# Kernel optimization log

Hardware: AMD Instinct MI355X
Metric: run time of the kernel (lower is better)

The kernel has to match this reference:

```python
import jax, jax.numpy as jnp
import numpy as np

B, S, DM, H, HD, M = 2, 1024, 1024, 16, 64, 32  # batch, seq, d_model, heads, head_dim, retrieved
EPS = 1e-5


def setup_inputs() -> dict:
    key = jax.random.key(0)
    ks = jax.random.split(key, 8)
    w = lambda k, shp: (jax.random.normal(k, shp) * 0.02).astype(jnp.float32)
    return {
        "previous_hidden": jax.random.normal(ks[0], (B, S, DM), jnp.float32),
        "mem_kv": jax.random.normal(ks[1], (B, S, M, 2, DM), jnp.float32),  # retrieved [k,v] from knn_memory.search
        "g_val": jax.random.uniform(ks[2], (1,), jnp.float32),
        "ln1_g": jnp.ones((DM,), jnp.float32), "ln1_b": jnp.zeros((DM,), jnp.float32),
        "c_attn_w": w(ks[3], (DM, 3 * DM)), "c_attn_b": jnp.zeros((3 * DM,), jnp.float32),
        "c_proj_w": w(ks[4], (DM, DM)), "c_proj_b": jnp.zeros((DM,), jnp.float32),
        "ln2_g": jnp.ones((DM,), jnp.float32), "ln2_b": jnp.zeros((DM,), jnp.float32),
        "fc_w": w(ks[5], (DM, 4 * DM)), "fc_b": jnp.zeros((4 * DM,), jnp.float32),
        "proj_w": w(ks[6], (4 * DM, DM)), "proj_b": jnp.zeros((DM,), jnp.float32),
    }


def _ln(x, g, b):
    m = jnp.mean(x, -1, keepdims=True)
    v = jnp.mean(jnp.square(x - m), -1, keepdims=True)
    return (x - m) * jax.lax.rsqrt(v + EPS) * g + b


def _split(t):  # [b,s,(h d)] -> [b,h,s,d]
    return t.reshape(B, S, H, HD).transpose(0, 2, 1, 3)


def _merge(t):  # [b,h,s,d] -> [b,s,(h d)]
    return t.transpose(0, 2, 1, 3).reshape(B, S, DM)


def _forward(previous_hidden, mem_kv, g_val, ln1_g, ln1_b, c_attn_w, c_attn_b,
             c_proj_w, c_proj_b, ln2_g, ln2_b, fc_w, fc_b, proj_w, proj_b):
    residual = previous_hidden
    h = _ln(previous_hidden, ln1_g, ln1_b)
    qkv = h @ c_attn_w + c_attn_b
    q, k, v = jnp.split(qkv, 3, axis=-1)
    q, k, v = _split(q), _split(k), _split(v)  # [b,h,s,d]

    # --- memory attention over retrieved k/v (per query position, M candidates) ---
    mem_k = mem_kv[..., 0, :].reshape(B, S, M, H, HD).transpose(0, 3, 1, 2, 4)  # [b,h,s,m,d]
    mem_v = mem_kv[..., 1, :].reshape(B, S, M, H, HD).transpose(0, 3, 1, 2, 4)
    mw = jnp.einsum('bhsd,bhsmd->bhsm', q, mem_k) / jnp.sqrt(jnp.asarray(HD, q.dtype))
    mw = jax.nn.softmax(mw, axis=-1)
    mem_attn_output = _merge(jnp.einsum('bhsm,bhsmd->bhsd', mw, mem_v))  # pre-c_proj (source overwrites c_proj'd output)

    # --- standard causal self-attention (GPT-2 block attn, incl. its c_proj) ---
    scores = jnp.einsum('bhqd,bhkd->bhqk', q, k) / jnp.sqrt(jnp.asarray(HD, q.dtype))
    causal = jnp.tril(jnp.ones((S, S), bool))
    scores = jnp.where(causal, scores, jnp.finfo(scores.dtype).min)
    p = jax.nn.softmax(scores, axis=-1)
    std_attn_output = _merge(jnp.einsum('bhqk,bhkd->bhqd', p, v)) @ c_proj_w + c_proj_b

    # gated combine (apply_linear_g=True, scalar g path since g_val.shape[0]==1)
    attn_output = (1.0 - g_val) * std_attn_output + g_val * mem_attn_output

    h = attn_output + residual
    residual2 = h
    h2 = _ln(h, ln2_g, ln2_b)
    ff = jax.nn.gelu(h2 @ fc_w + fc_b, approximate=True) @ proj_w + proj_b  # gelu_new
    return residual2 + ff


def reference(previous_hidden, mem_kv, g_val, ln1_g, ln1_b, c_attn_w, c_attn_b,
              c_proj_w, c_proj_b, ln2_g, ln2_b, fc_w, fc_b, proj_w, proj_b):
    return _forward(previous_hidden, mem_kv, g_val, ln1_g, ln1_b, c_attn_w, c_attn_b,
                    c_proj_w, c_proj_b, ln2_g, ln2_b, fc_w, fc_b, proj_w, proj_b)
```

## Files before the change

kernel.cpp:

```cpp
#include <hip/hip_runtime.h>


typedef short bf16x8 __attribute__((ext_vector_type(8)));
typedef float f32x4 __attribute__((ext_vector_type(4)));

__device__ __forceinline__ unsigned short f2b(float x) {
  unsigned int u = __float_as_uint(x);
  u += 0x7fffu + ((u >> 16) & 1u);
  return (unsigned short)(u >> 16);
}
__device__ __forceinline__ float b2f(unsigned int bits16) {
  return __uint_as_float(bits16 << 16);
}
__device__ __forceinline__ void async16(const void* g, void* l) {
  __builtin_amdgcn_global_load_lds((__attribute__((address_space(1))) void*)g,
                                   (__attribute__((address_space(3))) void*)l,
                                   16, 0, 0);
}

__global__ __launch_bounds__(256) void transpose_cast_kernel(
    const float* __restrict__ W, unsigned short* __restrict__ Wt, int K, int N) {
  __shared__ float tile[32][33];
  int n0 = blockIdx.x * 32, k0 = blockIdx.y * 32;
  int tx = threadIdx.x, ty = threadIdx.y;
#pragma unroll
  for (int i = 0; i < 4; i++)
    tile[ty + 8 * i][tx] = W[(size_t)(k0 + ty + 8 * i) * N + n0 + tx];
  __syncthreads();
#pragma unroll
  for (int i = 0; i < 4; i++)
    Wt[(size_t)(n0 + ty + 8 * i) * K + k0 + tx] = f2b(tile[tx][ty + 8 * i]);
}

__global__ __launch_bounds__(256) void ln_cast_kernel(
    const float* __restrict__ x, const float* __restrict__ gw,
    const float* __restrict__ bw, unsigned short* __restrict__ out) {
  int row = blockIdx.x, t = threadIdx.x;
  size_t base = (size_t)row * 1024 + t * 4;
  float4 v = *(const float4*)(x + base);
  float s = v.x + v.y + v.z + v.w;
  float q = v.x * v.x + v.y * v.y + v.z * v.z + v.w * v.w;
#pragma unroll
  for (int off = 32; off; off >>= 1) {
    s += __shfl_xor(s, off);
    q += __shfl_xor(q, off);
  }
  __shared__ float red[8];
  int w = t >> 6, l = t & 63;
  if (l == 0) { red[w] = s; red[w + 4] = q; }
  __syncthreads();
  s = red[0] + red[1] + red[2] + red[3];
  q = red[4] + red[5] + red[6] + red[7];
  float mean = s * (1.0f / 1024.0f);
  float var = q * (1.0f / 1024.0f) - mean * mean;
  float rstd = rsqrtf(var + 1e-5f);
  float4 g4 = *(const float4*)(gw + t * 4);
  float4 b4 = *(const float4*)(bw + t * 4);
  out[base + 0] = f2b((v.x - mean) * rstd * g4.x + b4.x);
  out[base + 1] = f2b((v.y - mean) * rstd * g4.y + b4.y);
  out[base + 2] = f2b((v.z - mean) * rstd * g4.z + b4.z);
  out[base + 3] = f2b((v.w - mean) * rstd * g4.w + b4.w);
}

template <int BM, int BN, int MODE>
__global__ __launch_bounds__(256, 2) void gemm_bf16(
    const unsigned short* __restrict__ A, const unsigned short* __restrict__ Bt,
    const float* __restrict__ bias, const float* __restrict__ res,
    void* __restrict__ outp, int N, int K) {
  constexpr int SM = BM / 32, SN = BN / 32;
  __shared__ __align__(16) unsigned short At[BM * 32];
  __shared__ __align__(16) unsigned short Bs[BN * 32];
  const int t = threadIdx.x, w = t >> 6, l = t & 63;
  const int wm = w >> 1, wn = w & 1;
  const int lq = l & 15, lk = l >> 4;
  const int m0 = blockIdx.y * BM, n0 = blockIdx.x * BN;
  const int lr = l >> 2, lc = l & 3;
  const unsigned short* Ag = A + (size_t)(m0 + w * 16 + lr) * K + lc * 8;
  const unsigned short* Bg = Bt + (size_t)(n0 + w * 16 + lr) * K + lc * 8;
  unsigned short* Al = &At[(size_t)t * 8];
  unsigned short* Bl = &Bs[(size_t)t * 8];
  f32x4 acc[SM][SN] = {};

  for (int k0 = 0; k0 < K; k0 += 32) {
#pragma unroll
    for (int p = 0; p < BM / 64; ++p)
      async16(Ag + (size_t)(p * 64) * K + k0, Al + p * 2048);
#pragma unroll
    for (int p = 0; p < BN / 64; ++p)
      async16(Bg + (size_t)(p * 64) * K + k0, Bl + p * 2048);
    __syncthreads();
    bf16x8 af[SM], bv[SN];
#pragma unroll
    for (int i = 0; i < SM; i++)
      af[i] = *(const bf16x8*)&At[(wm * (BM / 2) + i * 16 + lq) * 32 + lk * 8];
#pragma unroll
    for (int j = 0; j < SN; j++)
      bv[j] = *(const bf16x8*)&Bs[(wn * (BN / 2) + j * 16 + lq) * 32 + lk * 8];
#pragma unroll
    for (int i = 0; i < SM; i++)
#pragma unroll
      for (int j = 0; j < SN; j++)
        acc[i][j] = __builtin_amdgcn_mfma_f32_16x16x32_bf16(af[i], bv[j], acc[i][j], 0, 0, 0);
    __syncthreads();
  }

#pragma unroll
  for (int i = 0; i < SM; i++) {
    int mrow = m0 + wm * (BM / 2) + i * 16 + lk * 4;
#pragma unroll
    for (int j = 0; j < SN; j++) {
      int ncol = n0 + wn * (BN / 2) + j * 16 + lq;
      float bval = bias[ncol];
#pragma unroll
      for (int r = 0; r < 4; r++) {
        size_t idx = (size_t)(mrow + r) * N + ncol;
        float v = acc[i][j][r] + bval;
        if (MODE == 0) {
          ((unsigned short*)outp)[idx] = f2b(v);
        } else if (MODE == 1) {
          ((float*)outp)[idx] = v;
        } else if (MODE == 2) {
          float u = v + 0.044715f * v * v * v;
          float e = __expf(1.5957691216057308f * u);
          float th = 1.0f - 2.0f / (e + 1.0f);
          ((unsigned short*)outp)[idx] = f2b(0.5f * v * (1.0f + th));
        } else {
          ((float*)outp)[idx] = v + res[idx];
        }
      }
    }
  }
}

__global__ __launch_bounds__(512) void memattn_kernel(
    const unsigned short* __restrict__ qkv, const float* __restrict__ memkv,
    float* __restrict__ out) {
  int bs = blockIdx.x, t = threadIdx.x;
  __shared__ float qs[1024];
  __shared__ float wsm[512];
  {
    unsigned int u = *(const unsigned int*)(qkv + (size_t)bs * 3072 + t * 2);
    qs[t * 2] = b2f(u & 0xffffu);
    qs[t * 2 + 1] = b2f(u >> 16);
  }
  __syncthreads();
  int h = t >> 5, m = t & 31;
  const float* kp = memkv + (size_t)bs * 65536 + (size_t)m * 2048 + h * 64;
  float dot = 0.0f;
#pragma unroll
  for (int d4 = 0; d4 < 16; ++d4) {
    float4 kk = *(const float4*)(kp + d4 * 4);
    float4 q4 = *(const float4*)(&qs[h * 64 + d4 * 4]);
    dot += kk.x * q4.x + kk.y * q4.y + kk.z * q4.z + kk.w * q4.w;
  }
  dot *= 0.125f;
  float mx = dot;
#pragma unroll
  for (int off = 1; off < 32; off <<= 1) mx = fmaxf(mx, __shfl_xor(mx, off));
  float e = __expf(dot - mx);
  float sm = e;
#pragma unroll
  for (int off = 1; off < 32; off <<= 1) sm += __shfl_xor(sm, off);
  wsm[t] = e / sm;
  __syncthreads();
  const float* vbase = memkv + (size_t)bs * 65536 + 1024;
#pragma unroll
  for (int rep = 0; rep < 2; ++rep) {
    int eidx = t + rep * 512;
    int he = eidx >> 6;
    const float* wrow = &wsm[he * 32];
    float acc = 0.0f;
#pragma unroll
    for (int mm = 0; mm < 32; ++mm) acc += wrow[mm] * vbase[(size_t)mm * 2048 + eidx];
    out[(size_t)bs * 1024 + eidx] = acc;
  }
}

__global__ __launch_bounds__(256) void flash_kernel(
    const unsigned short* __restrict__ qkv, unsigned short* __restrict__ out) {
  int blk = blockIdx.x;
  int qt = blk & 15, bh = blk >> 4;
  int b = bh >> 4, h = bh & 15;
  int t = threadIdx.x, w = t >> 6, l = t & 63;
  int lq = l & 15, lk = l >> 4;
  __shared__ __align__(16) unsigned short Kt[32 * 72];
  __shared__ __align__(16) unsigned short Vt[64 * 40];
  __shared__ __align__(16) unsigned short Pb[4][16 * 40];

  const unsigned short* base = qkv + (size_t)b * 1024 * 3072;
  int qr0 = qt * 64 + w * 16;

  bf16x8 qf0 = *(const bf16x8*)(base + (size_t)(qr0 + lq) * 3072 + h * 64 + lk * 8);
  bf16x8 qf1 = *(const bf16x8*)(base + (size_t)(qr0 + lq) * 3072 + h * 64 + 32 + lk * 8);

  f32x4 o[4] = {};
  float mrow[4], lrow[4];
#pragma unroll
  for (int r = 0; r < 4; r++) { mrow[r] = -1e30f; lrow[r] = 0.0f; }

  int nch = (qt + 1) * 2;
  for (int c = 0; c < nch; ++c) {
    int kv0 = c * 32;
    {
      int rr = t >> 3, d8 = t & 7;
      const unsigned short* krow = base + (size_t)(kv0 + rr) * 3072 + 1024 + h * 64;
      *(bf16x8*)&Kt[rr * 72 + d8 * 8] = *(const bf16x8*)(krow + d8 * 8);
      bf16x8 v8 = *(const bf16x8*)(krow + 1024 + d8 * 8);
#pragma unroll
      for (int i = 0; i < 8; i++) Vt[(d8 * 8 + i) * 40 + rr] = (unsigned short)v8[i];
    }
    __syncthreads();

    f32x4 sv[2];
#pragma unroll
    for (int j = 0; j < 2; j++) {
      if (kv0 + j * 16 <= qr0 + 15) {
        bf16x8 k0f = *(const bf16x8*)&Kt[(j * 16 + lq) * 72 + lk * 8];
        bf16x8 k1f = *(const bf16x8*)&Kt[(j * 16 + lq) * 72 + 32 + lk * 8];
        f32x4 s = {};
        s = __builtin_amdgcn_mfma_f32_16x16x32_bf16(qf0, k0f, s, 0, 0, 0);
        s = __builtin_amdgcn_mfma_f32_16x16x32_bf16(qf1, k1f, s, 0, 0, 0);
#pragma unroll
        for (int r = 0; r < 4; r++) {
          float x = s[r] * 0.125f;
          int qrow = qr0 + lk * 4 + r;
          int kvg = kv0 + j * 16 + lq;
          if (kvg > qrow) x = -1e30f;
          s[r] = x;
        }
        sv[j] = s;
      } else {
        sv[j] = (f32x4){-1e30f, -1e30f, -1e30f, -1e30f};
      }
    }
#pragma unroll
    for (int r = 0; r < 4; r++) {
      float mnew = fmaxf(sv[0][r], sv[1][r]);
#pragma unroll
      for (int off = 1; off < 16; off <<= 1) mnew = fmaxf(mnew, __shfl_xor(mnew, off));
      mnew = fmaxf(mnew, mrow[r]);
      float a = __expf(mrow[r] - mnew);
      float e0 = __expf(sv[0][r] - mnew);
      float e1 = __expf(sv[1][r] - mnew);
      float rs = e0 + e1;
#pragma unroll
      for (int off = 1; off < 16; off <<= 1) rs += __shfl_xor(rs, off);
      lrow[r] = lrow[r] * a + rs;
      mrow[r] = mnew;
      o[0][r] *= a; o[1][r] *= a; o[2][r] *= a; o[3][r] *= a;
      Pb[w][(lk * 4 + r) * 40 + lq] = f2b(e0);
      Pb[w][(lk * 4 + r) * 40 + 16 + lq] = f2b(e1);
    }
    __syncthreads();

    if (kv0 <= qr0 + 15) {
      bf16x8 pf = *(const bf16x8*)&Pb[w][lq * 40 + lk * 8];
#pragma unroll
      for (int dt = 0; dt < 4; dt++) {
        bf16x8 vf = *(const bf16x8*)&Vt[(dt * 16 + lq) * 40 + lk * 8];
        o[dt] = __builtin_amdgcn_mfma_f32_16x16x32_bf16(pf, vf, o[dt], 0, 0, 0);
      }
    }
    __syncthreads();
  }

  unsigned short* op = out + (size_t)b * 1024 * 1024 + h * 64;
#pragma unroll
  for (int dt = 0; dt < 4; dt++)
#pragma unroll
    for (int r = 0; r < 4; r++) {
      float v = o[dt][r] / lrow[r];
      op[(size_t)(qr0 + lk * 4 + r) * 1024 + dt * 16 + lq] = f2b(v);
    }
}

__global__ __launch_bounds__(256) void combine_ln2_kernel(
    const float* __restrict__ stdp, const float* __restrict__ mem,
    const float* __restrict__ resid, const float* __restrict__ gval,
    const float* __restrict__ gw, const float* __restrict__ bw,
    float* __restrict__ hmid, unsigned short* __restrict__ h2) {
  int row = blockIdx.x, t = threadIdx.x;
  float g = gval[0];
  size_t base = (size_t)row * 1024 + t * 4;
  float4 a = *(const float4*)(stdp + base);
  float4 m4 = *(const float4*)(mem + base);
  float4 r4 = *(const float4*)(resid + base);
  float4 hv;
  hv.x = (1.0f - g) * a.x + g * m4.x + r4.x;
  hv.y = (1.0f - g) * a.y + g * m4.y + r4.y;
  hv.z = (1.0f - g) * a.z + g * m4.z + r4.z;
  hv.w = (1.0f - g) * a.w + g * m4.w + r4.w;
  *(float4*)(hmid + base) = hv;
  float s = hv.x + hv.y + hv.z + hv.w;
  float q = hv.x * hv.x + hv.y * hv.y + hv.z * hv.z + hv.w * hv.w;
#pragma unroll
  for (int off = 32; off; off >>= 1) {
    s += __shfl_xor(s, off);
    q += __shfl_xor(q, off);
  }
  __shared__ float red[8];
  int w = t >> 6, l = t & 63;
  if (l == 0) { red[w] = s; red[w + 4] = q; }
  __syncthreads();
  s = red[0] + red[1] + red[2] + red[3];
  q = red[4] + red[5] + red[6] + red[7];
  float mean = s * (1.0f / 1024.0f);
  float var = q * (1.0f / 1024.0f) - mean * mean;
  float rstd = rsqrtf(var + 1e-5f);
  float4 g4 = *(const float4*)(gw + t * 4);
  float4 b4 = *(const float4*)(bw + t * 4);
  h2[base + 0] = f2b((hv.x - mean) * rstd * g4.x + b4.x);
  h2[base + 1] = f2b((hv.y - mean) * rstd * g4.y + b4.y);
  h2[base + 2] = f2b((hv.z - mean) * rstd * g4.z + b4.z);
  h2[base + 3] = f2b((hv.w - mean) * rstd * g4.w + b4.w);
}

extern "C" void kernel_launch(void* const* d_in, const int* in_sizes, int n_in,
                              void* d_out, int out_size, void* d_ws, size_t ws_size,
                              hipStream_t stream) {
  const float* prev = (const float*)d_in[0];
  const float* memkv = (const float*)d_in[1];
  const float* gval = (const float*)d_in[2];
  const float* ln1g = (const float*)d_in[3];
  const float* ln1b = (const float*)d_in[4];
  const float* attw = (const float*)d_in[5];
  const float* attb = (const float*)d_in[6];
  const float* cpw = (const float*)d_in[7];
  const float* cpb = (const float*)d_in[8];
  const float* ln2g = (const float*)d_in[9];
  const float* ln2b = (const float*)d_in[10];
  const float* fcw = (const float*)d_in[11];
  const float* fcb = (const float*)d_in[12];
  const float* pjw = (const float*)d_in[13];
  const float* pjb = (const float*)d_in[14];

  char* ws = (char*)d_ws;
  size_t off = 0;
  unsigned short* wqkv_t = (unsigned short*)(ws + off); off += (size_t)3072 * 1024 * 2;
  unsigned short* wcp_t  = (unsigned short*)(ws + off); off += (size_t)1024 * 1024 * 2;
  unsigned short* wfc_t  = (unsigned short*)(ws + off); off += (size_t)4096 * 1024 * 2;
  unsigned short* wpj_t  = (unsigned short*)(ws + off); off += (size_t)1024 * 4096 * 2;
  unsigned short* h_bf   = (unsigned short*)(ws + off); off += (size_t)2048 * 1024 * 2;
  unsigned short* qkv_bf = (unsigned short*)(ws + off); off += (size_t)2048 * 3072 * 2;
  unsigned short* satt_bf= (unsigned short*)(ws + off); off += (size_t)2048 * 1024 * 2;
  unsigned short* h2_bf  = (unsigned short*)(ws + off); off += (size_t)2048 * 1024 * 2;
  float* matt  = (float*)(ws + off); off += (size_t)2048 * 1024 * 4;
  float* sproj = (float*)(ws + off); off += (size_t)2048 * 1024 * 4;
  float* hmid  = (float*)(ws + off); off += (size_t)2048 * 1024 * 4;
  unsigned short* ff1_bf = (unsigned short*)(ws + off); off += (size_t)2048 * 4096 * 2;

  dim3 tb(32, 8);
  transpose_cast_kernel<<<dim3(3072 / 32, 1024 / 32), tb, 0, stream>>>(attw, wqkv_t, 1024, 3072);
  transpose_cast_kernel<<<dim3(1024 / 32, 1024 / 32), tb, 0, stream>>>(cpw, wcp_t, 1024, 1024);
  transpose_cast_kernel<<<dim3(4096 / 32, 1024 / 32), tb, 0, stream>>>(fcw, wfc_t, 1024, 4096);
  transpose_cast_kernel<<<dim3(1024 / 32, 4096 / 32), tb, 0, stream>>>(pjw, wpj_t, 4096, 1024);

  ln_cast_kernel<<<2048, 256, 0, stream>>>(prev, ln1g, ln1b, h_bf);

  gemm_bf16<128, 128, 0><<<dim3(24, 16), 256, 0, stream>>>(h_bf, wqkv_t, attb, nullptr, qkv_bf, 3072, 1024);

  memattn_kernel<<<2048, 512, 0, stream>>>(qkv_bf, memkv, matt);
  flash_kernel<<<512, 256, 0, stream>>>(qkv_bf, satt_bf);

  gemm_bf16<128, 64, 1><<<dim3(16, 16), 256, 0, stream>>>(satt_bf, wcp_t, cpb, nullptr, sproj, 1024, 1024);

  combine_ln2_kernel<<<2048, 256, 0, stream>>>(sproj, matt, prev, gval, ln2g, ln2b, hmid, h2_bf);

  gemm_bf16<128, 128, 2><<<dim3(32, 16), 256, 0, stream>>>(h2_bf, wfc_t, fcb, nullptr, ff1_bf, 4096, 1024);

  gemm_bf16<128, 64, 3><<<dim3(16, 16), 256, 0, stream>>>(ff1_bf, wpj_t, pjb, hmid, (float*)d_out, 1024, 4096);
}
```

Baseline: 1.059 ms.

## Widen GEMM K-tile with XOR-swizzled LDS, restructure mem-attn, swizzle flash V

The GEMM now stages 64-wide K tiles, which halves the number of barrier pairs, and XOR-swizzles the LDS layout to avoid bank conflicts. Memory attention loads q into registers and computes dots with coalesced contiguous K reads plus shuffle reductions instead of a strided per-(head,m) layout. The flash kernel processes the longest causal query tiles first and swizzles the V transpose in LDS to cut bank conflicts. These are several unrelated changes, and the larger LDS footprint may reduce GEMM occupancy.

Measured after the change: 968.2 us. 8.5% less time.

```diff
diff --git a/kernel.cpp b/kernel.cpp
--- a/kernel.cpp
+++ b/kernel.cpp
@@ -68,39 +68,45 @@
     const float* __restrict__ bias, const float* __restrict__ res,
     void* __restrict__ outp, int N, int K) {
   constexpr int SM = BM / 32, SN = BN / 32;
-  __shared__ __align__(16) unsigned short At[BM * 32];
-  __shared__ __align__(16) unsigned short Bs[BN * 32];
+  __shared__ __align__(16) unsigned short At[BM * 64];
+  __shared__ __align__(16) unsigned short Bs[BN * 64];
   const int t = threadIdx.x, w = t >> 6, l = t & 63;
   const int wm = w >> 1, wn = w & 1;
   const int lq = l & 15, lk = l >> 4;
   const int m0 = blockIdx.y * BM, n0 = blockIdx.x * BN;
-  const int lr = l >> 2, lc = l & 3;
-  const unsigned short* Ag = A + (size_t)(m0 + w * 16 + lr) * K + lc * 8;
-  const unsigned short* Bg = Bt + (size_t)(n0 + w * 16 + lr) * K + lc * 8;
+  const int sr = t >> 3;
+  const int scs = (t & 7) ^ (sr & 7);
+  const unsigned short* Ag = A + (size_t)(m0 + sr) * K + scs * 8;
+  const unsigned short* Bg = Bt + (size_t)(n0 + sr) * K + scs * 8;
   unsigned short* Al = &At[(size_t)t * 8];
   unsigned short* Bl = &Bs[(size_t)t * 8];
+  const int swr = (lq & 7) << 3;
   f32x4 acc[SM][SN] = {};
 
-  for (int k0 = 0; k0 < K; k0 += 32) {
-#pragma unroll
-    for (int p = 0; p < BM / 64; ++p)
-      async16(Ag + (size_t)(p * 64) * K + k0, Al + p * 2048);
-#pragma unroll
-    for (int p = 0; p < BN / 64; ++p)
-      async16(Bg + (size_t)(p * 64) * K + k0, Bl + p * 2048);
-    __syncthreads();
-    bf16x8 af[SM], bv[SN];
-#pragma unroll
-    for (int i = 0; i < SM; i++)
-      af[i] = *(const bf16x8*)&At[(wm * (BM / 2) + i * 16 + lq) * 32 + lk * 8];
-#pragma unroll
-    for (int j = 0; j < SN; j++)
-      bv[j] = *(const bf16x8*)&Bs[(wn * (BN / 2) + j * 16 + lq) * 32 + lk * 8];
-#pragma unroll
-    for (int i = 0; i < SM; i++)
+  for (int k0 = 0; k0 < K; k0 += 64) {
+#pragma unroll
+    for (int p = 0; p < BM / 32; ++p)
+      async16(Ag + (size_t)(p * 32) * K + k0, Al + p * 2048);
+#pragma unroll
+    for (int p = 0; p < BN / 32; ++p)
+      async16(Bg + (size_t)(p * 32) * K + k0, Bl + p * 2048);
+    __syncthreads();
+#pragma unroll
+    for (int kk = 0; kk < 2; ++kk) {
+      const int koff = (kk * 32 + lk * 8) ^ swr;
+      bf16x8 af[SM], bv[SN];
+#pragma unroll
+      for (int i = 0; i < SM; i++)
+        af[i] = *(const bf16x8*)&At[(wm * (BM / 2) + i * 16 + lq) * 64 + koff];
 #pragma unroll
       for (int j = 0; j < SN; j++)
-        acc[i][j] = __builtin_amdgcn_mfma_f32_16x16x32_bf16(af[i], bv[j], acc[i][j], 0, 0, 0);
+        bv[j] = *(const bf16x8*)&Bs[(wn * (BN / 2) + j * 16 + lq) * 64 + koff];
+#pragma unroll
+      for (int i = 0; i < SM; i++)
+#pragma unroll
+        for (int j = 0; j < SN; j++)
+          acc[i][j] = __builtin_amdgcn_mfma_f32_16x16x32_bf16(af[i], bv[j], acc[i][j], 0, 0, 0);
+    }
     __syncthreads();
   }
 
@@ -136,32 +142,47 @@
     const unsigned short* __restrict__ qkv, const float* __restrict__ memkv,
     float* __restrict__ out) {
   int bs = blockIdx.x, t = threadIdx.x;
-  __shared__ float qs[1024];
+  __shared__ float dotb[16 * 33];
   __shared__ float wsm[512];
+  int w = t >> 6, l = t & 63;
+  const unsigned short* qp = qkv + (size_t)bs * 3072 + l * 16;
+  bf16x8 qa = *(const bf16x8*)qp;
+  bf16x8 qb = *(const bf16x8*)(qp + 8);
+  float qreg[16];
+#pragma unroll
+  for (int i = 0; i < 8; i++) {
+    qreg[i] = b2f((unsigned short)qa[i]);
+    qreg[8 + i] = b2f((unsigned short)qb[i]);
+  }
+  const float* kbase = memkv + (size_t)bs * 65536 + (size_t)l * 16;
+#pragma unroll
+  for (int j = 0; j < 4; j++) {
+    int m = w * 4 + j;
+    const float* kp = kbase + (size_t)m * 2048;
+    float dot = 0.0f;
+#pragma unroll
+    for (int d4 = 0; d4 < 4; d4++) {
+      float4 kk = *(const float4*)(kp + d4 * 4);
+      dot += kk.x * qreg[d4 * 4 + 0] + kk.y * qreg[d4 * 4 + 1] +
+             kk.z * qreg[d4 * 4 + 2] + kk.w * qreg[d4 * 4 + 3];
+    }
+    dot += __shfl_xor(dot, 1);
+    dot += __shfl_xor(dot, 2);
+    if ((l & 3) == 0) dotb[(l >> 2) * 33 + m] = dot * 0.125f;
+  }
+  __syncthreads();
   {
-    unsigned int u = *(const unsigned int*)(qkv + (size_t)bs * 3072 + t * 2);
-    qs[t * 2] = b2f(u & 0xffffu);
-    qs[t * 2 + 1] = b2f(u >> 16);
-  }
-  __syncthreads();
-  int h = t >> 5, m = t & 31;
-  const float* kp = memkv + (size_t)bs * 65536 + (size_t)m * 2048 + h * 64;
-  float dot = 0.0f;
-#pragma unroll
-  for (int d4 = 0; d4 < 16; ++d4) {
-    float4 kk = *(const float4*)(kp + d4 * 4);
-    float4 q4 = *(const float4*)(&qs[h * 64 + d4 * 4]);
-    dot += kk.x * q4.x + kk.y * q4.y + kk.z * q4.z + kk.w * q4.w;
-  }
-  dot *= 0.125f;
-  float mx = dot;
-#pragma unroll
-  for (int off = 1; off < 32; off <<= 1) mx = fmaxf(mx, __shfl_xor(mx, off));
-  float e = __expf(dot - mx);
-  float sm = e;
-#pragma unroll
-  for (int off = 1; off < 32; off <<= 1) sm += __shfl_xor(sm, off);
-  wsm[t] = e / sm;
+    int h = t >> 5, m = t & 31;
+    float d = dotb[h * 33 + m];
+    float mx = d;
+#pragma unroll
+    for (int off = 1; off < 32; off <<= 1) mx = fmaxf(mx, __shfl_xor(mx, off));
+    float e = __expf(d - mx);
+    float sm = e;
+#pragma unroll
+    for (int off = 1; off < 32; off <<= 1) sm += __shfl_xor(sm, off);
+    wsm[t] = e / sm;
+  }
   __syncthreads();
   const float* vbase = memkv + (size_t)bs * 65536 + 1024;
 #pragma unroll
@@ -179,7 +200,7 @@
 __global__ __launch_bounds__(256) void flash_kernel(
     const unsigned short* __restrict__ qkv, unsigned short* __restrict__ out) {
   int blk = blockIdx.x;
-  int qt = blk & 15, bh = blk >> 4;
+  int qt = 15 - (blk & 15), bh = blk >> 4;
   int b = bh >> 4, h = bh & 15;
   int t = threadIdx.x, w = t >> 6, l = t & 63;
   int lq = l & 15, lk = l >> 4;
@@ -206,8 +227,9 @@
       const unsigned short* krow = base + (size_t)(kv0 + rr) * 3072 + 1024 + h * 64;
       *(bf16x8*)&Kt[rr * 72 + d8 * 8] = *(const bf16x8*)(krow + d8 * 8);
       bf16x8 v8 = *(const bf16x8*)(krow + 1024 + d8 * 8);
-#pragma unroll
-      for (int i = 0; i < 8; i++) Vt[(d8 * 8 + i) * 40 + rr] = (unsigned short)v8[i];
+      int vc = rr ^ ((d8 & 3) << 3);
+#pragma unroll
+      for (int i = 0; i < 8; i++) Vt[(d8 * 8 + i) * 40 + vc] = (unsigned short)v8[i];
     }
     __syncthreads();
 
@@ -257,7 +279,8 @@
       bf16x8 pf = *(const bf16x8*)&Pb[w][lq * 40 + lk * 8];
 #pragma unroll
       for (int dt = 0; dt < 4; dt++) {
-        bf16x8 vf = *(const bf16x8*)&Vt[(dt * 16 + lq) * 40 + lk * 8];
+        int s = (dt * 2 + (lq >> 3)) & 3;
+        bf16x8 vf = *(const bf16x8*)&Vt[(dt * 16 + lq) * 40 + ((lk ^ s) << 3)];
         o[dt] = __builtin_amdgcn_mfma_f32_16x16x32_bf16(pf, vf, o[dt], 0, 0, 0);
       }
     }
```
